# Optimization experiments

Measured on AMD Instinct MI355X. Metric: run time of the kernel, lower is better.

## Reference

```python
import jax, jax.numpy as jnp
import numpy as np

B, S, HID = 1, 2048, 7168
QLORA = 1536
NH = 32          # index_n_heads
HD = 128         # index_head_dim
ROPE = 64        # qk_rope_head_dim
TOPK = 512       # index_topk
EPS = 1e-6
NEG = -1e9       # finite mask value -> deterministic top-k (no -inf ties)


def _rope(x, cos, sin):
    # non-interleaved rotary: x [b,s,h,d]; cos/sin [s, d//2]
    half = x.shape[-1] // 2
    x1, x2 = x[..., :half], x[..., half:]
    c = cos[None, :, None, :]
    s = sin[None, :, None, :]
    return jnp.concatenate([x1 * c - x2 * s, x1 * s + x2 * c], axis=-1)


def setup_inputs() -> dict:
    key = jax.random.key(0)
    ks = jax.random.split(key, 8)
    x = jax.random.normal(ks[0], (B, S, HID), jnp.float32)
    qr = jax.random.normal(ks[1], (B, S, QLORA), jnp.float32)
    # rotary tables, theta=10000
    inv = 1.0 / (10000.0 ** (np.arange(0, ROPE, 2, dtype=np.float32) / ROPE))
    ang = np.arange(S, dtype=np.float32)[:, None] * inv[None, :]   # [S, ROPE//2]
    freqs_cos = jnp.asarray(np.cos(ang))
    freqs_sin = jnp.asarray(np.sin(ang))
    # causal additive mask [S, S], broadcasts over batch on [b,t,s]
    tri = jnp.tril(jnp.ones((S, S), jnp.bool_))
    mask = jnp.where(tri, 0.0, NEG).astype(jnp.float32)
    wq_b = jax.random.normal(ks[2], (QLORA, NH * HD), jnp.float32) / np.sqrt(QLORA)
    wk = jax.random.normal(ks[3], (HID, HD), jnp.float32) / np.sqrt(HID)
    k_norm_w = jnp.ones((HD,), jnp.float32)
    w_weights = jax.random.normal(ks[4], (HID, NH), jnp.float32) / np.sqrt(HID)
    return {"x": x, "qr": qr, "freqs_cos": freqs_cos, "freqs_sin": freqs_sin,
            "mask": mask, "wq_b": wq_b, "wk": wk, "k_norm_w": k_norm_w,
            "w_weights": w_weights}


def reference(x, qr, freqs_cos, freqs_sin, mask, wq_b, wk, k_norm_w, w_weights):
    b, s, _ = x.shape
    # queries
    q = (qr @ wq_b).reshape(b, s, NH, HD)
    q_pe, q_nope = q[..., :ROPE], q[..., ROPE:]
    q_pe = _rope(q_pe, freqs_cos, freqs_sin)
    q = jnp.concatenate([q_pe, q_nope], axis=-1)            # [b,s,NH,HD]
    # keys: project + RMSNorm + rope on first ROPE dims
    k = x @ wk                                              # [b,s,HD]
    var = jnp.mean(k * k, axis=-1, keepdims=True)
    k = k_norm_w * (k * jax.lax.rsqrt(var + EPS))
    k_pe, k_nope = k[..., :ROPE], k[..., ROPE:]
    k_pe = _rope(k_pe[:, :, None, :], freqs_cos, freqs_sin)[:, :, 0, :]
    k = jnp.concatenate([k_pe, k_nope], axis=-1)            # [b,s,HD]
    # per-head query weights
    weights = (x @ w_weights) * (NH ** -0.5) * (HD ** -0.5)  # [b,s,NH]
    # relu scores and per-head weighted reduction
    logits = jax.nn.relu(jnp.einsum('bthd,bsd->btsh', q, k))  # [b,t,s,NH]
    score = jnp.einsum('btsh,bth->bts', logits, weights) + mask
    # top-k token selection -> additive index mask
    topk_idx = jax.lax.top_k(score, min(TOPK, s))[1]          # [b,t,k]
    bi = jnp.arange(b)[:, None, None]
    ti = jnp.arange(s)[None, :, None]
    out = jnp.full((b, s, s), -jnp.inf, dtype=x.dtype)
    out = out.at[bi, ti, topk_idx].set(0.0)
    return out
```

## Files before the change

### kernel.cpp

```cpp
#include <hip/hip_runtime.h>
#include <hip/hip_bf16.h>
#include <math.h>

#define S_LEN 2048
#define HID   7168
#define QLORA 1536
#define NH    32
#define HD    128
#define T0    512
#define MROWS 1536
#define NEGV  -1000000000.0f
#define EPSV  1e-6f
#define NEG_FILL -3.0e38f
#define KSPLIT 16
#define KCHUNK 448

typedef __attribute__((ext_vector_type(8))) short bf16x8;
typedef __attribute__((ext_vector_type(4))) float f32x4;

__device__ __forceinline__ unsigned short f2bf(float x) {
    __hip_bfloat16 h = __float2bfloat16(x);
    union { __hip_bfloat16 h; unsigned short u; } cv; cv.h = h; return cv.u;
}
__device__ __forceinline__ float bf2f(short u) {
    return __uint_as_float(((unsigned)(unsigned short)u) << 16);
}
__device__ __forceinline__ void gload_lds16(const void* gsrc, void* ldst) {
    __builtin_amdgcn_global_load_lds(
        (const __attribute__((address_space(1))) void*)gsrc,
        (__attribute__((address_space(3))) void*)ldst,
        16, 0, 0);
}

__global__ __launch_bounds__(256) void transpose_wqb(
    const float* __restrict__ B, unsigned short* __restrict__ BT)
{
    __shared__ float tbuf[64][65];
    const int tid = threadIdx.x;
    const int n0 = blockIdx.x * 64;
    const int k0 = blockIdx.y * 64;
    {
        int r = tid >> 2, c0 = (tid & 3) * 16;
        const float* src = &B[(size_t)(k0 + r) * 4096 + n0 + c0];
        #pragma unroll
        for (int i = 0; i < 4; ++i) {
            float4 v = *(const float4*)(src + 4 * i);
            tbuf[r][c0 + 4 * i]     = v.x;
            tbuf[r][c0 + 4 * i + 1] = v.y;
            tbuf[r][c0 + 4 * i + 2] = v.z;
            tbuf[r][c0 + 4 * i + 3] = v.w;
        }
    }
    __syncthreads();
    {
        int nn = tid >> 2, ks = (tid & 3) * 16;
        bf16x8 p0, p1;
        #pragma unroll
        for (int j = 0; j < 8; ++j) {
            p0[j] = (short)f2bf(tbuf[ks + j][nn]);
            p1[j] = (short)f2bf(tbuf[ks + 8 + j][nn]);
        }
        unsigned short* dst = &BT[(size_t)(n0 + nn) * QLORA + k0 + ks];
        *(bf16x8*)dst       = p0;
        *(bf16x8*)(dst + 8) = p1;
    }
}

__global__ __launch_bounds__(256) void transpose_w(
    const float* __restrict__ wk, const float* __restrict__ ww,
    unsigned short* __restrict__ wbT)
{
    __shared__ float tbuf[64][33];
    const int tid = threadIdx.x;
    const int k0 = blockIdx.x * 64;
    const int nt = blockIdx.y;
    const float* src; int ld, nc0;
    if (nt < 4) { src = wk; ld = HD; nc0 = nt * 32; }
    else        { src = ww; ld = NH; nc0 = 0; }
    {
        int r = tid >> 2, c0 = (tid & 3) * 8;
        const float* sp = &src[(size_t)(k0 + r) * ld + nc0 + c0];
        #pragma unroll
        for (int i = 0; i < 2; ++i) {
            float4 v = *(const float4*)(sp + 4 * i);
            tbuf[r][c0 + 4 * i]     = v.x;
            tbuf[r][c0 + 4 * i + 1] = v.y;
            tbuf[r][c0 + 4 * i + 2] = v.z;
            tbuf[r][c0 + 4 * i + 3] = v.w;
        }
    }
    __syncthreads();
    {
        int nn = tid >> 3, ks = (tid & 7) * 8;
        bf16x8 p;
        #pragma unroll
        for (int j = 0; j < 8; ++j) p[j] = (short)f2bf(tbuf[ks + j][nn]);
        *(bf16x8*)&wbT[(size_t)(nt * 32 + nn) * HID + k0 + ks] = p;
    }
}

__global__ __launch_bounds__(256) void cast_qr(
    const float* __restrict__ qr, unsigned short* __restrict__ qrb)
{
    int idx = blockIdx.x * 256 + threadIdx.x;
    const float* src = qr + (size_t)T0 * QLORA + (size_t)idx * 8;
    float4 f0 = *(const float4*)src;
    float4 f1 = *(const float4*)(src + 4);
    bf16x8 p;
    p[0]=(short)f2bf(f0.x); p[1]=(short)f2bf(f0.y); p[2]=(short)f2bf(f0.z); p[3]=(short)f2bf(f0.w);
    p[4]=(short)f2bf(f1.x); p[5]=(short)f2bf(f1.y); p[6]=(short)f2bf(f1.z); p[7]=(short)f2bf(f1.w);
    *(bf16x8*)(qrb + (size_t)idx * 8) = p;
}

__global__ __launch_bounds__(256) void kw_gemm2(
    const float* __restrict__ x, const unsigned short* __restrict__ wbT,
    unsigned short* __restrict__ P)
{
    __shared__ char As[2][4096];
    __shared__ char Bs[2][10240];
    const int tid = threadIdx.x;
    const int bid = blockIdx.x;
    const int wg = (bid & 7) * 64 + (bid >> 3);
    const int kc = wg >> 5;
    const int m0 = (wg & 31) * 64;
    const int kbase = kc * KCHUNK;
    const int wv = tid >> 6, l = tid & 63, g = l >> 4, r15 = l & 15;
    const int ar = tid >> 2, asub = tid & 3;
    f32x4 acc[10] = {};
    float4 fa, fb;

#define LOAD_A(kt) do {                                                          \
        const float* ap = &x[(size_t)(m0 + ar) * HID + kbase + (kt) * 32 + asub * 8]; \
        fa = *(const float4*)ap;  fb = *(const float4*)(ap + 4);                 \
    } while (0)
#define WRITE_A(buf) do {                                                        \
        bf16x8 pk;                                                               \
        pk[0]=(short)f2bf(fa.x); pk[1]=(short)f2bf(fa.y);                        \
        pk[2]=(short)f2bf(fa.z); pk[3]=(short)f2bf(fa.w);                        \
        pk[4]=(short)f2bf(fb.x); pk[5]=(short)f2bf(fb.y);                        \
        pk[6]=(short)f2bf(fb.z); pk[7]=(short)f2bf(fb.w);                        \
        *(bf16x8*)(As[buf] + (ar << 6) + ((asub ^ ((ar >> 1) & 3)) << 4)) = pk;  \
    } while (0)
#define STAGE_B(buf, kt) do {                                                    \
        int k0_ = kbase + (kt) * 32;                                             \
        { int slot = (wv << 6) + l;                                              \
          int n_ = slot >> 2, sub_ = (slot & 3) ^ ((n_ >> 1) & 3);               \
          gload_lds16(wbT + (size_t)n_ * HID + k0_ + sub_ * 8,                   \
                      Bs[buf] + (wv << 10)); }                                   \
        { int slot = 256 + (wv << 6) + l;                                        \
          int n_ = slot >> 2, sub_ = (slot & 3) ^ ((n_ >> 1) & 3);               \
          gload_lds16(wbT + (size_t)n_ * HID + k0_ + sub_ * 8,                   \
                      Bs[buf] + 4096 + (wv << 10)); }                            \
        if (wv < 2) {                                                            \
          int slot = 512 + (wv << 6) + l;                                        \
          int n_ = slot >> 2, sub_ = (slot & 3) ^ ((n_ >> 1) & 3);               \
          gload_lds16(wbT + (size_t)n_ * HID + k0_ + sub_ * 8,                   \
                      Bs[buf] + 8192 + (wv << 10)); }                            \
    } while (0)

    LOAD_A(0);
    STAGE_B(0, 0);
    WRITE_A(0);
    __syncthreads();
    int cur = 0;
    for (int t = 0; t < 14; ++t) {
        if (t < 13) { LOAD_A(t + 1); STAGE_B(cur ^ 1, t + 1); }
        {
            char* Ab = As[cur];
            char* Bb = Bs[cur];
            int ra = (wv << 4) + r15;
            bf16x8 a = *(const bf16x8*)(Ab + (ra << 6) + ((g ^ ((ra >> 1) & 3)) << 4));
            #pragma unroll
            for (int fn = 0; fn < 10; ++fn) {
                int nb = (fn << 4) + r15;
                bf16x8 b = *(const bf16x8*)(Bb + (nb << 6) + ((g ^ ((nb >> 1) & 3)) << 4));
                acc[fn] = __builtin_amdgcn_mfma_f32_16x16x32_bf16(a, b, acc[fn], 0, 0, 0);
            }
        }
        if (t < 13) WRITE_A(cur ^ 1);
        __syncthreads();
        cur ^= 1;
    }
#undef LOAD_A
#undef WRITE_A
#undef STAGE_B
    #pragma unroll
    for (int fn = 0; fn < 10; ++fn)
        #pragma unroll
        for (int rr = 0; rr < 4; ++rr) {
            int row = m0 + (wv << 4) + (g << 2) + rr;
            P[((size_t)kc * S_LEN + row) * 160 + (fn << 4) + r15] = f2bf(acc[fn][rr]);
        }
}

__global__ __launch_bounds__(512) void kw_finish16(
    const unsigned short* __restrict__ P, const float* __restrict__ knw,
    const float* __restrict__ fcos, const float* __restrict__ fsin,
    unsigned short* __restrict__ Kf, float* __restrict__ W)
{
    __shared__ float res[16][160];
    __shared__ float rsq[16];
    const int tid = threadIdx.x;
    const int stile = blockIdx.x;
    const int row0 = stile * 16;
    const int r = tid >> 5, j = tid & 31;

    #pragma unroll
    for (int jj = 0; jj < 5; ++jj) {
        int c = j + 32 * jj;
        float s = 0.f;
        #pragma unroll
        for (int kc = 0; kc < KSPLIT; ++kc)
            s += bf2f((short)P[(size_t)(kc * S_LEN + row0 + r) * 160 + c]);
        res[r][c] = s;
    }
    __syncthreads();
    {
        float s2 = 0.f;
        #pragma unroll
        for (int cg = 0; cg < 4; ++cg) { float v = res[r][cg * 32 + j]; s2 += v * v; }
        #pragma unroll
        for (int off = 16; off > 0; off >>= 1) s2 += __shfl_xor(s2, off, 32);
        if (j == 0) rsq[r] = rsqrtf(s2 * (1.0f / 128.0f) + EPSV);
    }
    __syncthreads();
    {
        int rr = tid >> 5, h = tid & 31;
        W[(size_t)(row0 + rr) * NH + h] = res[rr][128 + h] * 0.015625f;
    }
    if (tid < 256) {
        int ks = tid >> 6, l = tid & 63;
        int row = l & 15, g = l >> 4;
        int t = row0 + row;
        float rs = rsq[row];
        bf16x8 pack;
        #pragma unroll
        for (int jj2 = 0; jj2 < 8; ++jj2) {
            int d = ks * 32 + 8 * g + jj2;
            float v;
            if (d < 32) {
                float a = res[row][d]      * rs * knw[d];
                float b = res[row][d + 32] * rs * knw[d + 32];
                v = a * fcos[(size_t)t * 32 + d] - b * fsin[(size_t)t * 32 + d];
            } else if (d < 64) {
                int jx = d - 32;
                float a = res[row][jx] * rs * knw[jx];
                float b = res[row][d]  * rs * knw[d];
                v = a * fsin[(size_t)t * 32 + jx] + b * fcos[(size_t)t * 32 + jx];
            } else {
                v = res[row][d] * rs * knw[d];
            }
            pack[jj2] = (short)f2bf(v);
        }
        *(bf16x8*)&Kf[(size_t)stile * 2048 + ks * 512 + l * 8] = pack;
    }
}

__global__ __launch_bounds__(256) void gemm_q2(
    const unsigned short* __restrict__ qrb, const unsigned short* __restrict__ wqbT,
    unsigned short* __restrict__ Qbu)
{
    __shared__ char lds[2][12288];
    const int tid = threadIdx.x;
    const int bid = blockIdx.x;
    const int wg = (bid & 7) * 96 + (bid >> 3);
    const int n0 = (wg / 24) * 128;
    const int m0 = (wg % 24) * 64;
    const int wv = tid >> 6, l = tid & 63, g = l >> 4, r15 = l & 15;
    const int lrow = l >> 2, lsub = l & 3;
    const int wm = wv >> 1, wn = wv & 1;
    f32x4 acc[2][4] = {};

#define STAGE_Q(buf, kt) do {                                                   \
        int k0_ = (kt) * 32;                                                    \
        { int row_ = wv * 16 + lrow; int gs_ = lsub ^ ((row_ >> 1) & 3);        \
          gload_lds16(qrb + (size_t)(m0 + row_) * QLORA + k0_ + gs_ * 8,        \
                      lds[buf] + (wv << 10)); }                                 \
        { int row_ = wv * 32 + lrow; int gs_ = lsub ^ ((row_ >> 1) & 3);        \
          gload_lds16(wqbT + (size_t)(n0 + row_) * QLORA + k0_ + gs_ * 8,       \
                      lds[buf] + 4096 + (wv << 11)); }                          \
        { int row_ = wv * 32 + 16 + lrow; int gs_ = lsub ^ ((row_ >> 1) & 3);   \
          gload_lds16(wqbT + (size_t)(n0 + row_) * QLORA + k0_ + gs_ * 8,       \
                      lds[buf] + 4096 + (wv << 11) + 1024); }                   \
    } while (0)

    STAGE_Q(0, 0);
    __syncthreads();
    int cur = 0;
    for (int t = 0; t < 48; ++t) {
        if (t + 1 < 48) STAGE_Q(cur ^ 1, t + 1);
        char* As = lds[cur];
        char* Bs = lds[cur] + 4096;
        bf16x8 a[2], b[4];
        #pragma unroll
        for (int fm = 0; fm < 2; ++fm) {
            int ra = wm * 32 + fm * 16 + r15;
            a[fm] = *(const bf16x8*)(As + (ra << 6) + ((g ^ ((ra >> 1) & 3)) << 4));
        }
        #pragma unroll
        for (int fn = 0; fn < 4; ++fn) {
            int nb = wn * 64 + fn * 16 + r15;
            b[fn] = *(const bf16x8*)(Bs + (nb << 6) + ((g ^ ((nb >> 1) & 3)) << 4));
        }
        #pragma unroll
        for (int fm = 0; fm < 2; ++fm)
            #pragma unroll
            for (int fn = 0; fn < 4; ++fn)
                acc[fm][fn] = __builtin_amdgcn_mfma_f32_16x16x32_bf16(a[fm], b[fn], acc[fm][fn], 0, 0, 0);
        __syncthreads();
        cur ^= 1;
    }
#undef STAGE_Q
    #pragma unroll
    for (int fm = 0; fm < 2; ++fm)
        #pragma unroll
        for (int fn = 0; fn < 4; ++fn)
            #pragma unroll
            for (int rr = 0; rr < 4; ++rr) {
                int row = m0 + wm * 32 + fm * 16 + 4 * g + rr;
                int col = n0 + wn * 64 + fn * 16 + r15;
                Qbu[(size_t)row * 4096 + col] = f2bf(acc[fm][fn][rr]);
            }
}

__global__ __launch_bounds__(512, 1) void score_mfma(
    const unsigned short* __restrict__ Qb, const unsigned short* __restrict__ Kf,
    const float* __restrict__ W, const float* __restrict__ fcos,
    const float* __restrict__ fsin, float* __restrict__ sc)
{
    __shared__ unsigned short QsU[32 * 16 * 128];
    __shared__ float wl2[512];
    char* qsb = (char*)QsU;
    const int tid = threadIdx.x;
    const int bid = blockIdx.x;
    const int sp  = blockIdx.y;
    const int t0 = T0 + 16 * bid;
    const int m0 = 16 * bid;

    #pragma unroll
    for (int i = 0; i < 16; ++i) {
        int slot = tid + i * 512;
        int h   = slot >> 8;
        int row = (slot >> 4) & 15;
        int d0  = (slot & 15) * 8;
        const unsigned short* qrow = Qb + (size_t)(m0 + row) * 4096 + h * 128;
        bf16x8 mainv = *(const bf16x8*)(qrow + d0);
        bf16x8 pack;
        if (d0 < 64) {
            bf16x8 part = *(const bf16x8*)(qrow + d0 + ((d0 < 32) ? 32 : -32));
            int j0 = d0 & 31;
            const float* cp = &fcos[(size_t)(t0 + row) * 32 + j0];
            const float* sp2 = &fsin[(size_t)(t0 + row) * 32 + j0];
            #pragma unroll
            for (int jj = 0; jj < 8; ++jj) {
                float f = bf2f(mainv[jj]);
                float p = bf2f(part[jj]);
                float c = cp[jj], s = sp2[jj];
                float v = (d0 < 32) ? (f * c - p * s) : (p * s + f * c);
                pack[jj] = (short)f2bf(v);
            }
        } else {
            pack = mainv;
        }
        int byte = ((h << 12) + (row << 8) + (d0 << 1)) ^ ((row & 7) << 4);
        *(bf16x8*)(qsb + byte) = pack;
    }
    {
        int h = tid >> 4, g = (tid >> 2) & 3, r = tid & 3;
        wl2[tid] = W[(size_t)(t0 + 4 * g + r) * NH + h];
    }
    __syncthreads();

    const int l    = tid & 63;
    const int g    = l >> 4;
    const int arow = l & 15;
    const int sw   = (l & 7) << 4;
    const int wv   = tid >> 6;
    const int nst  = 33 + bid;

    for (int stile = sp + 4 * wv; stile < nst; stile += 32) {
        bf16x8 kf[4];
        #pragma unroll
        for (int ks = 0; ks < 4; ++ks)
            kf[ks] = *(const bf16x8*)&Kf[(size_t)stile * 2048 + ks * 512 + l * 8];
        f32x4 score = {0.f, 0.f, 0.f, 0.f};
        #pragma unroll 4
        for (int h = 0; h < 32; ++h) {
            f32x4 acc = {0.f, 0.f, 0.f, 0.f};
            const int hb = h << 12;
            #pragma unroll
            for (int ks = 0; ks < 4; ++ks) {
                int off = hb + (arow << 8) + ks * 64 + (g << 4);
                bf16x8 af = *(const bf16x8*)(qsb + (off ^ sw));
                acc = __builtin_amdgcn_mfma_f32_16x16x32_bf16(af, kf[ks], acc, 0, 0, 0);
            }
            f32x4 w4 = *(const f32x4*)&wl2[(h << 4) + (g << 2)];
            #pragma unroll
            for (int r = 0; r < 4; ++r)
                score[r] += fmaxf(acc[r], 0.f) * w4[r];
        }
        #pragma unroll
        for (int r = 0; r < 4; ++r) {
            int t = t0 + 4 * g + r;
            int s = stile * 16 + (l & 15);
            sc[(size_t)(t - T0) * S_LEN + s] = (s <= t) ? score[r] : NEGV;
        }
    }
}

__global__ __launch_bounds__(256) void topk_row(
    const float* __restrict__ sc, float* __restrict__ out)
{
    __shared__ float scl[S_LEN];
    __shared__ unsigned int hist[256];
    __shared__ unsigned int wtot[4];
    __shared__ unsigned int sh_prefix;
    __shared__ int sh_krem;
    const int tid = threadIdx.x;
    const int lane = tid & 63, wvi = tid >> 6;
    const int qrow = blockIdx.x;
    const int t = T0 + qrow;
    const float* srow = sc + (size_t)qrow * S_LEN;

    for (int i = tid; i < S_LEN; i += 256) {
        float v = srow[i];
        scl[i] = (i <= t) ? v : NEGV;
    }
    __syncthreads();
    unsigned int* u = (unsigned int*)scl;
    #pragma unroll
    for (int jj = 0; jj < 8; ++jj) {
        int i = tid * 8 + jj;
        unsigned int b = __float_as_uint(scl[i]);
        u[i] = (b & 0x80000000u) ? ~b : (b | 0x80000000u);
    }
    if (tid == 0) { sh_prefix = 0u; sh_krem = 512; }
    __syncthreads();

    #pragma unroll
    for (int pass = 0; pass < 4; ++pass) {
        const int shift = 24 - 8 * pass;
        hist[tid] = 0u;
        __syncthreads();
        unsigned int pfx = sh_prefix;
        #pragma unroll
        for (int jj = 0; jj < 8; ++jj) {
            unsigned int uv = u[tid * 8 + jj];
            bool ok = (pass == 0) || ((uv >> (shift + 8)) == (pfx >> (shift + 8)));
            if (ok) atomicAdd(&hist[(uv >> shift) & 255u], 1u);
        }
        __syncthreads();
        unsigned int v = hist[tid];
        unsigned int s = v;
        #pragma unroll
        for (int off = 1; off < 64; off <<= 1) {
            unsigned int t2 = __shfl_down(s, off, 64);
            if (lane + off < 64) s += t2;
        }
        if (lane == 0) wtot[wvi] = s;
        int krem = sh_krem;
        __syncthreads();
        unsigned int S = s;
        #pragma unroll
        for (int w = 0; w < 4; ++w)
            if (w > wvi) S += wtot[w];
        if ((int)S >= krem && (int)(S - v) < krem) {
            sh_krem = krem - (int)(S - v);
            sh_prefix = pfx | ((unsigned int)tid << shift);
        }
        __syncthreads();
    }

    const unsigned int uthr = sh_prefix;
    const int krem = sh_krem;
    int ec = 0;
    #pragma unroll
    for (int jj = 0; jj < 8; ++jj) ec += (u[tid * 8 + jj] == uthr) ? 1 : 0;
    unsigned int c = (unsigned int)ec;
    unsigned int p = c;
    #pragma unroll
    for (int off = 1; off < 64; off <<= 1) {
        unsigned int t2 = __shfl_up(p, off, 64);
        if (lane >= off) p += t2;
    }
    if (lane == 63) wtot[wvi] = p;
    __syncthreads();
    unsigned int add = 0;
    #pragma unroll
    for (int w = 0; w < 4; ++w)
        if (w < wvi) add += wtot[w];
    int base = (int)(p - c + add);

    float* orow = out + (size_t)t * S_LEN;
    float o[8];
    #pragma unroll
    for (int jj = 0; jj < 8; ++jj) {
        unsigned int uv = u[tid * 8 + jj];
        bool sel;
        if (uv > uthr) { sel = true; }
        else if (uv == uthr) { sel = (base < krem); base++; }
        else { sel = false; }
        o[jj] = sel ? 0.0f : NEG_FILL;
    }
    float4 o0 = {o[0], o[1], o[2], o[3]};
    float4 o1 = {o[4], o[5], o[6], o[7]};
    *(float4*)&orow[tid * 8]     = o0;
    *(float4*)&orow[tid * 8 + 4] = o1;
}

__global__ __launch_bounds__(256) void fill_low(float* __restrict__ out)
{
    int idx = blockIdx.x * 256 + threadIdx.x;
    if (idx >= (T0 * S_LEN) / 4) return;
    int col4 = idx & 511;
    float v = (col4 < 128) ? 0.0f : NEG_FILL;
    float4 o = {v, v, v, v};
    ((float4*)out)[idx] = o;
}

extern "C" void kernel_launch(void* const* d_in, const int* in_sizes, int n_in,
                              void* d_out, int out_size, void* d_ws, size_t ws_size,
                              hipStream_t stream)
{
    (void)in_sizes; (void)n_in; (void)out_size; (void)ws_size;
    const float* x    = (const float*)d_in[0];
    const float* qr   = (const float*)d_in[1];
    const float* fcos = (const float*)d_in[2];
    const float* fsin = (const float*)d_in[3];
    const float* wq_b = (const float*)d_in[5];
    const float* wk   = (const float*)d_in[6];
    const float* knw  = (const float*)d_in[7];
    const float* ww   = (const float*)d_in[8];
    float* out = (float*)d_out;
    char*  wsb = (char*)d_ws;

    unsigned short* Kf   = (unsigned short*)wsb;
    float*          W    = (float*)(wsb + 512 * 1024);
    char*           reg1 = wsb + 768 * 1024;
    char*           reg2 = reg1 + 12582912;
    unsigned short* wbT  = (unsigned short*)reg1;
    unsigned short* Qbu  = (unsigned short*)reg1;
    unsigned short* P    = (unsigned short*)reg2;
    unsigned short* wqbT = (unsigned short*)reg2;
    float*          sc   = (float*)reg2;
    unsigned short* qrb  = (unsigned short*)d_out;

    transpose_w   <<<dim3(112, 5), 256, 0, stream>>>(wk, ww, wbT);
    kw_gemm2      <<<512, 256,        0, stream>>>(x, wbT, P);
    kw_finish16   <<<128, 512,        0, stream>>>(P, knw, fcos, fsin, Kf, W);
    transpose_wqb <<<dim3(64, 24), 256, 0, stream>>>(wq_b, wqbT);
    cast_qr       <<<1152, 256,       0, stream>>>(qr, qrb);
    gemm_q2       <<<768, 256,        0, stream>>>(qrb, wqbT, Qbu);
    score_mfma    <<<dim3(96, 4), 512,  0, stream>>>(Qbu, Kf, W, fcos, fsin, sc);
    topk_row      <<<MROWS, 256,      0, stream>>>(sc, out);
    fill_low      <<<(T0 * S_LEN / 4 + 255) / 256, 256, 0, stream>>>(out);
}
```

Before: 162.3 us.

## Fuse query RoPE into GEMM epilogue and split score heads across waves

Query rotary embedding now runs in the gemm_q2 epilogue on fp32 accumulators, so the score kernel no longer rotates and stages Q through LDS. The score kernel is rewritten so each of 4 waves holds 8 heads of Q fragments in registers. The waves jointly process each key tile, and their partial weighted scores are reduced through a small LDS buffer with barriers. Blocks are reversed so the longest causal rows start first, and 256-thread blocks allow two per CU. This trades one LDS staging pass for many more registers and two barriers per tile.

```diff
diff --git a/kernel.cpp b/kernel.cpp
--- a/kernel.cpp
+++ b/kernel.cpp
@@ -258,6 +258,7 @@
 
 __global__ __launch_bounds__(256) void gemm_q2(
     const unsigned short* __restrict__ qrb, const unsigned short* __restrict__ wqbT,
+    const float* __restrict__ fcos, const float* __restrict__ fsin,
     unsigned short* __restrict__ Qbu)
 {
     __shared__ char lds[2][12288];
@@ -311,6 +312,23 @@
         cur ^= 1;
     }
 #undef STAGE_Q
+    if (wn == 0) {
+        #pragma unroll
+        for (int fm = 0; fm < 2; ++fm)
+            #pragma unroll
+            for (int rr = 0; rr < 4; ++rr) {
+                int t = T0 + m0 + wm * 32 + fm * 16 + 4 * g + rr;
+                #pragma unroll
+                for (int p = 0; p < 2; ++p) {
+                    int jj = p * 16 + r15;
+                    float c = fcos[(size_t)t * 32 + jj];
+                    float s = fsin[(size_t)t * 32 + jj];
+                    float a = acc[fm][p][rr], b = acc[fm][p + 2][rr];
+                    acc[fm][p][rr]     = a * c - b * s;
+                    acc[fm][p + 2][rr] = a * s + b * c;
+                }
+            }
+    }
     #pragma unroll
     for (int fm = 0; fm < 2; ++fm)
         #pragma unroll
@@ -323,88 +341,62 @@
             }
 }
 
-__global__ __launch_bounds__(512, 1) void score_mfma(
+__global__ __launch_bounds__(256, 2) void score_mfma2(
     const unsigned short* __restrict__ Qb, const unsigned short* __restrict__ Kf,
-    const float* __restrict__ W, const float* __restrict__ fcos,
-    const float* __restrict__ fsin, float* __restrict__ sc)
-{
-    __shared__ unsigned short QsU[32 * 16 * 128];
-    __shared__ float wl2[512];
-    char* qsb = (char*)QsU;
-    const int tid = threadIdx.x;
-    const int bid = blockIdx.x;
+    const float* __restrict__ W, float* __restrict__ sc)
+{
+    __shared__ float ps[4][320];
+    __shared__ float wl2[32][16];
+    const int tid = threadIdx.x;
+    const int tt  = 95 - blockIdx.x;
     const int sp  = blockIdx.y;
-    const int t0 = T0 + 16 * bid;
-    const int m0 = 16 * bid;
-
-    #pragma unroll
-    for (int i = 0; i < 16; ++i) {
-        int slot = tid + i * 512;
-        int h   = slot >> 8;
-        int row = (slot >> 4) & 15;
-        int d0  = (slot & 15) * 8;
-        const unsigned short* qrow = Qb + (size_t)(m0 + row) * 4096 + h * 128;
-        bf16x8 mainv = *(const bf16x8*)(qrow + d0);
-        bf16x8 pack;
-        if (d0 < 64) {
-            bf16x8 part = *(const bf16x8*)(qrow + d0 + ((d0 < 32) ? 32 : -32));
-            int j0 = d0 & 31;
-            const float* cp = &fcos[(size_t)(t0 + row) * 32 + j0];
-            const float* sp2 = &fsin[(size_t)(t0 + row) * 32 + j0];
-            #pragma unroll
-            for (int jj = 0; jj < 8; ++jj) {
-                float f = bf2f(mainv[jj]);
-                float p = bf2f(part[jj]);
-                float c = cp[jj], s = sp2[jj];
-                float v = (d0 < 32) ? (f * c - p * s) : (p * s + f * c);
-                pack[jj] = (short)f2bf(v);
-            }
-        } else {
-            pack = mainv;
-        }
-        int byte = ((h << 12) + (row << 8) + (d0 << 1)) ^ ((row & 7) << 4);
-        *(bf16x8*)(qsb + byte) = pack;
-    }
-    {
-        int h = tid >> 4, g = (tid >> 2) & 3, r = tid & 3;
-        wl2[tid] = W[(size_t)(t0 + 4 * g + r) * NH + h];
-    }
-    __syncthreads();
-
-    const int l    = tid & 63;
-    const int g    = l >> 4;
-    const int arow = l & 15;
-    const int sw   = (l & 7) << 4;
-    const int wv   = tid >> 6;
-    const int nst  = 33 + bid;
-
-    for (int stile = sp + 4 * wv; stile < nst; stile += 32) {
+    const int t0  = T0 + 16 * tt;
+    const int wv  = tid >> 6, l = tid & 63, g = l >> 4, r15 = l & 15;
+
+    for (int i = tid; i < 512; i += 256) {
+        int h = i >> 4, gg = (i >> 2) & 3, r = i & 3;
+        wl2[h][gg * 4 + r] = W[(size_t)(t0 + 4 * gg + r) * NH + h];
+    }
+    bf16x8 qf[8][4];
+    {
+        const unsigned short* qbase = Qb + (size_t)(16 * tt + r15) * 4096 + g * 8;
+        #pragma unroll
+        for (int hh = 0; hh < 8; ++hh)
+            #pragma unroll
+            for (int ks = 0; ks < 4; ++ks)
+                qf[hh][ks] = *(const bf16x8*)(qbase + (8 * wv + hh) * 128 + ks * 32);
+    }
+    __syncthreads();
+
+    const int nst = 33 + tt;
+    for (int stile = sp; stile < nst; stile += 4) {
         bf16x8 kf[4];
         #pragma unroll
         for (int ks = 0; ks < 4; ++ks)
             kf[ks] = *(const bf16x8*)&Kf[(size_t)stile * 2048 + ks * 512 + l * 8];
         f32x4 score = {0.f, 0.f, 0.f, 0.f};
-        #pragma unroll 4
-        for (int h = 0; h < 32; ++h) {
+        #pragma unroll
+        for (int hh = 0; hh < 8; ++hh) {
             f32x4 acc = {0.f, 0.f, 0.f, 0.f};
-            const int hb = h << 12;
-            #pragma unroll
-            for (int ks = 0; ks < 4; ++ks) {
-                int off = hb + (arow << 8) + ks * 64 + (g << 4);
-                bf16x8 af = *(const bf16x8*)(qsb + (off ^ sw));
-                acc = __builtin_amdgcn_mfma_f32_16x16x32_bf16(af, kf[ks], acc, 0, 0, 0);
-            }
-            f32x4 w4 = *(const f32x4*)&wl2[(h << 4) + (g << 2)];
+            #pragma unroll
+            for (int ks = 0; ks < 4; ++ks)
+                acc = __builtin_amdgcn_mfma_f32_16x16x32_bf16(qf[hh][ks], kf[ks], acc, 0, 0, 0);
+            f32x4 w4 = *(const f32x4*)&wl2[8 * wv + hh][g * 4];
             #pragma unroll
             for (int r = 0; r < 4; ++r)
                 score[r] += fmaxf(acc[r], 0.f) * w4[r];
         }
         #pragma unroll
-        for (int r = 0; r < 4; ++r) {
-            int t = t0 + 4 * g + r;
-            int s = stile * 16 + (l & 15);
-            sc[(size_t)(t - T0) * S_LEN + s] = (s <= t) ? score[r] : NEGV;
-        }
+        for (int r = 0; r < 4; ++r) ps[wv][l * 5 + r] = score[r];
+        __syncthreads();
+        {
+            float v = ((ps[0][l * 5 + wv] + ps[1][l * 5 + wv])
+                       + ps[2][l * 5 + wv]) + ps[3][l * 5 + wv];
+            int t = t0 + 4 * g + wv;
+            int s = stile * 16 + r15;
+            sc[(size_t)(t - T0) * S_LEN + s] = (s <= t) ? v : NEGV;
+        }
+        __syncthreads();
     }
 }
 
@@ -550,8 +542,8 @@
     kw_finish16   <<<128, 512,        0, stream>>>(P, knw, fcos, fsin, Kf, W);
     transpose_wqb <<<dim3(64, 24), 256, 0, stream>>>(wq_b, wqbT);
     cast_qr       <<<1152, 256,       0, stream>>>(qr, qrb);
-    gemm_q2       <<<768, 256,        0, stream>>>(qrb, wqbT, Qbu);
-    score_mfma    <<<dim3(96, 4), 512,  0, stream>>>(Qbu, Kf, W, fcos, fsin, sc);
+    gemm_q2       <<<768, 256,        0, stream>>>(qrb, wqbT, fcos, fsin, Qbu);
+    score_mfma2   <<<dim3(96, 4), 256,  0, stream>>>(Qbu, Kf, W, sc);
     topk_row      <<<MROWS, 256,      0, stream>>>(sc, out);
     fill_low      <<<(T0 * S_LEN / 4 + 255) / 256, 256, 0, stream>>>(out);
 }
```

Measured after the change: 159.3 us. Within noise of the previous version (-1.8%).
